# Performance work log

Measured on AMD Instinct MI355X. Metric: run time of the kernel, lower is better.

The kernel has to match this reference:

```python
import jax, jax.numpy as jnp
import numpy as np

EPSILON = 1e-6          # SwitchGate epsilon
CV_EPS = 1e-10          # cv_squared epsilon
CAPACITY_FACTOR = 1.0


def cv_squared(v):
    # torch: x.float().var() is unbiased (ddof=1) over the flattened tensor
    v = v.astype(jnp.float32).ravel()
    m = v.mean()
    return jnp.var(v, ddof=1) / (m * m + CV_EPS)


def setup_inputs() -> dict:
    key = jax.random.key(0)
    k1, k2 = jax.random.split(key, 2)
    B, N, D, E = 2048, 128, 512, 64
    x = jax.random.normal(k1, (B, N, D), dtype=jnp.float32)
    # nn.Linear(dim, num_experts): weight [E, D], bias [E]
    lim = 1.0 / (D ** 0.5)
    w_gate = jax.random.uniform(k2, (E, D), dtype=jnp.float32, minval=-lim, maxval=lim)
    b_gate = jnp.zeros((E,), dtype=jnp.float32)
    return {"x": x, "w_gate": w_gate, "b_gate": b_gate}


def reference(x, w_gate, b_gate):
    B, N, _ = x.shape
    E = w_gate.shape[0]
    capacity = int(CAPACITY_FACTOR * B)  # static

    logits = jnp.einsum('bnd,ed->bne', x, w_gate) + b_gate      # [B,N,E]
    gate_scores = jax.nn.softmax(logits, axis=-1)

    # topk(1, dim=-1) -> indices [B,N,1]
    _, idx = jax.lax.top_k(gate_scores, 1)

    # torch scatter_(dim=1, idx, 1): mask[b, idx[b,n,0], 0] = 1
    # (scatter along the SEQ dim with expert indices, faithful to source)
    bi = jnp.arange(B)[:, None]                                  # [B,1]
    mask = jnp.zeros_like(gate_scores).at[bi, idx[:, :, 0], 0].set(1.0)

    masked = gate_scores * mask                                  # [B,N,E]
    denom = masked.sum(axis=0, keepdims=True) + EPSILON          # [1,N,E]
    gs = masked / denom * capacity                               # [B,N,E]

    importance = gs.sum(axis=0)                                  # [N,E]
    load = (gs > 0).sum(axis=0)                                  # [N,E] int
    loss = cv_squared(importance) + cv_squared(load)
    return gs, loss
```

## Files before the change

kernel.cpp:

```cpp
#include <hip/hip_runtime.h>
#include <hip/hip_bf16.h>
#include <stdint.h>

#define Bb 2048
#define Nn 128
#define Dd 512
#define Ee 64
#define Mm (Bb * Nn)

typedef __bf16 bf16t;
typedef bf16t bf16x8 __attribute__((ext_vector_type(8)));
typedef float f32x4 __attribute__((ext_vector_type(4)));

union AFrag { bf16x8 v; uint32_t d[4]; };
union BFrag { bf16x8 v; uint4 q; };

__global__ __launch_bounds__(256) void k_packw(const float* __restrict__ w,
                                               uint16_t* __restrict__ whi,
                                               uint16_t* __restrict__ wlo) {
  int i = blockIdx.x * 256 + threadIdx.x;
  if (i < Ee * Dd) {
    float v = w[i];
    uint32_t ub = __float_as_uint(v);
    uint32_t h = ub >> 16;
    float rest = v - __uint_as_float(h << 16);
    whi[i] = (uint16_t)h;
    wlo[i] = (uint16_t)(__float_as_uint(rest) >> 16);
  }
}

__global__ __launch_bounds__(256) void k_main(const float* __restrict__ x,
    const uint16_t* __restrict__ whi, const uint16_t* __restrict__ wlo,
    const float* __restrict__ bg,
    float* __restrict__ out, float* __restrict__ gate0, int* __restrict__ amax)
{
  int tid = threadIdx.x;
  int wave = tid >> 6, lane = tid & 63;
  int l15 = lane & 15, quad = lane >> 4;

  {
    float4 z = make_float4(0.f, 0.f, 0.f, 0.f);
    float4* ob = (float4*)(out) + (size_t)blockIdx.x * 1024;
    #pragma unroll
    for (int i = 0; i < 4; ++i) ob[tid + 256 * i] = z;
  }

  size_t p0 = (size_t)blockIdx.x * 64 + (size_t)wave * 16;
  const float* xrow = x + (p0 + (size_t)l15) * Dd + quad * 8;

  f32x4 acc[4];
  #pragma unroll
  for (int ct = 0; ct < 4; ++ct) acc[ct] = (f32x4){0.f, 0.f, 0.f, 0.f};

  for (int kt = 0; kt < Dd; kt += 32) {
    float4 a0 = *(const float4*)(xrow + kt);
    float4 a1 = *(const float4*)(xrow + kt + 4);
    float av[8] = {a0.x, a0.y, a0.z, a0.w, a1.x, a1.y, a1.z, a1.w};
    AFrag ahi, alo;
    #pragma unroll
    for (int j = 0; j < 4; ++j) {
      uint32_t u0 = __float_as_uint(av[2 * j]);
      uint32_t u1 = __float_as_uint(av[2 * j + 1]);
      uint32_t h0 = u0 >> 16, h1 = u1 >> 16;
      float r0 = av[2 * j]     - __uint_as_float(h0 << 16);
      float r1 = av[2 * j + 1] - __uint_as_float(h1 << 16);
      uint32_t lo0 = __float_as_uint(r0) >> 16;
      uint32_t lo1 = __float_as_uint(r1) >> 16;
      ahi.d[j] = h0 | (h1 << 16);
      alo.d[j] = lo0 | (lo1 << 16);
    }
    #pragma unroll
    for (int ct = 0; ct < 4; ++ct) {
      int c = ct * 16 + l15;
      BFrag bh, bl;
      bh.q = *(const uint4*)(whi + (size_t)c * Dd + kt + quad * 8);
      bl.q = *(const uint4*)(wlo + (size_t)c * Dd + kt + quad * 8);
      acc[ct] = __builtin_amdgcn_mfma_f32_16x16x32_bf16(ahi.v, bh.v, acc[ct], 0, 0, 0);
      acc[ct] = __builtin_amdgcn_mfma_f32_16x16x32_bf16(ahi.v, bl.v, acc[ct], 0, 0, 0);
      acc[ct] = __builtin_amdgcn_mfma_f32_16x16x32_bf16(alo.v, bh.v, acc[ct], 0, 0, 0);
    }
  }

  float bia[4];
  #pragma unroll
  for (int ct = 0; ct < 4; ++ct) bia[ct] = bg[ct * 16 + l15];

  #pragma unroll
  for (int reg = 0; reg < 4; ++reg) {
    float v[4];
    #pragma unroll
    for (int ct = 0; ct < 4; ++ct) v[ct] = acc[ct][reg] + bia[ct];

    float mx = v[0]; int mi = l15;
    #pragma unroll
    for (int ct = 1; ct < 4; ++ct) {
      int c = ct * 16 + l15;
      if (v[ct] > mx) { mx = v[ct]; mi = c; }
    }
    #pragma unroll
    for (int off = 1; off < 16; off <<= 1) {
      float om = __shfl_xor(mx, off);
      int   oi = __shfl_xor(mi, off);
      if (om > mx || (om == mx && oi < mi)) { mx = om; mi = oi; }
    }
    float s = 0.f;
    #pragma unroll
    for (int ct = 0; ct < 4; ++ct) s += expf(v[ct] - mx);
    #pragma unroll
    for (int off = 1; off < 16; off <<= 1) s += __shfl_xor(s, off);

    if (l15 == 0) {
      size_t pr = p0 + (size_t)quad * 4 + reg;
      gate0[pr] = expf(v[0] - mx) / s;
      amax[pr]  = mi;
    }
  }
}

__global__ __launch_bounds__(64) void k_cov(const int* __restrict__ amax,
                                            const float* __restrict__ gate0,
                                            unsigned long long* __restrict__ covbits,
                                            float* __restrict__ covg) {
  int b = blockIdx.x;
  int lane = threadIdx.x;
  __shared__ int idxs[Nn];
  idxs[lane]      = amax[(size_t)b * Nn + lane];
  idxs[lane + 64] = amax[(size_t)b * Nn + 64 + lane];
  __syncthreads();
  bool cov = false;
  #pragma unroll 8
  for (int n = 0; n < Nn; ++n) cov |= (idxs[n] == lane);
  unsigned long long bits = __ballot(cov);
  if (lane == 0) covbits[b] = bits;
  covg[(size_t)b * Ee + lane] = cov ? gate0[(size_t)b * Nn + lane] : 0.f;
}

__global__ __launch_bounds__(256) void k_reduce(const float* __restrict__ covg,
                                                const unsigned long long* __restrict__ covbits,
                                                float* __restrict__ denomS,
                                                float* __restrict__ cntS) {
  int e = blockIdx.x;
  int t = threadIdx.x;
  float s = 0.f, c = 0.f;
  for (int b = t; b < Bb; b += 256) {
    s += covg[(size_t)b * Ee + e];
    c += (float)((covbits[b] >> e) & 1ull);
  }
  #pragma unroll
  for (int off = 1; off < 64; off <<= 1) {
    s += __shfl_xor(s, off);
    c += __shfl_xor(c, off);
  }
  __shared__ float ss[4], cs[4];
  int wave = t >> 6, lane = t & 63;
  if (lane == 0) { ss[wave] = s; cs[wave] = c; }
  __syncthreads();
  if (t == 0) {
    float S = 0.f, C = 0.f;
    #pragma unroll
    for (int i = 0; i < 4; ++i) { S += ss[i]; C += cs[i]; }
    denomS[e] = S;
    cntS[e] = C;
  }
}

__global__ __launch_bounds__(64) void k_scatter(const float* __restrict__ gate0,
                                                const unsigned long long* __restrict__ covbits,
                                                const float* __restrict__ denomS,
                                                float* __restrict__ out) {
  int b = blockIdx.x;
  int n = threadIdx.x;
  if ((covbits[b] >> n) & 1ull) {
    float g = gate0[(size_t)b * Nn + n];
    out[((size_t)(b * Nn + n)) * Ee] = g * 2048.0f / (denomS[n] + 1e-6f);
  }
}

__global__ __launch_bounds__(64) void k_loss(const float* __restrict__ denomS,
                                             const float* __restrict__ cntS,
                                             float* __restrict__ out) {
  int lane = threadIdx.x;
  double S = (double)denomS[lane];
  double imp = S / (S + 1e-6) * 2048.0;
  double ld = (double)cntS[lane];
  double s1i = imp, s2i = imp * imp, s1l = ld, s2l = ld * ld;
  #pragma unroll
  for (int off = 1; off < 64; off <<= 1) {
    s1i += __shfl_xor(s1i, off);
    s2i += __shfl_xor(s2i, off);
    s1l += __shfl_xor(s1l, off);
    s2l += __shfl_xor(s2l, off);
  }
  if (lane == 0) {
    const double Nt = (double)(Nn * Ee);
    double mi_ = s1i / Nt;
    double vi  = (s2i - Nt * mi_ * mi_) / (Nt - 1.0);
    double li  = vi / (mi_ * mi_ + 1e-10);
    double ml_ = s1l / Nt;
    double vl  = (s2l - Nt * ml_ * ml_) / (Nt - 1.0);
    double ll_ = vl / (ml_ * ml_ + 1e-10);
    out[(size_t)Mm * Ee] = (float)(li + ll_);
  }
}

extern "C" void kernel_launch(void* const* d_in, const int* in_sizes, int n_in,
                              void* d_out, int out_size, void* d_ws, size_t ws_size,
                              hipStream_t stream) {
  const float* x  = (const float*)d_in[0];
  const float* w  = (const float*)d_in[1];
  const float* bg = (const float*)d_in[2];
  float* out = (float*)d_out;

  char* ws = (char*)d_ws;
  float* gate0 = (float*)ws;
  int*   amax  = (int*)(ws + (size_t)Mm * 4);
  unsigned long long* covbits =
      (unsigned long long*)(ws + (size_t)Mm * 8);
  float* denomS = (float*)(ws + (size_t)Mm * 8 + (size_t)Bb * 8);
  float* cntS   = denomS + Ee;
  uint16_t* whi = (uint16_t*)(denomS + 2 * Ee);
  uint16_t* wlo = whi + Ee * Dd;
  float* covg   = (float*)(wlo + Ee * Dd);

  k_packw<<<(Ee * Dd + 255) / 256, 256, 0, stream>>>(w, whi, wlo);
  k_main<<<Mm / 64, 256, 0, stream>>>(x, whi, wlo, bg, out, gate0, amax);
  k_cov<<<Bb, 64, 0, stream>>>(amax, gate0, covbits, covg);
  k_reduce<<<Ee, 256, 0, stream>>>(covg, covbits, denomS, cntS);
  k_scatter<<<Bb, 64, 0, stream>>>(gate0, covbits, denomS, out);
  k_loss<<<1, 64, 0, stream>>>(denomS, cntS, out);
}
```

Before: 882.5 us.

## Tile four row groups per wave, reuse weight fragments, prefetch next x slice

Each wave now handles 64 rows (four 16-row tiles) instead of 16, so each weight hi/lo fragment loaded from global memory feeds four tiles of MFMAs. The x loads for the next k-step are software-prefetched into registers while the current step computes, and the fp32-to-bf16 hi/lo split uses byte-permute instructions. The grid shrinks by four and each block zeroes four times more output. Register pressure rises (16 accumulators plus prefetch buffers), which may lower occupancy. With only 1024 blocks, there is less parallelism for hiding the latency of this memory-bound x stream.

```diff
diff --git a/kernel.cpp b/kernel.cpp
--- a/kernel.cpp
+++ b/kernel.cpp
@@ -14,6 +14,14 @@
 
 union AFrag { bf16x8 v; uint32_t d[4]; };
 union BFrag { bf16x8 v; uint4 q; };
+
+__device__ __forceinline__ void split2(float f0, float f1, uint32_t& hi, uint32_t& lo) {
+  uint32_t u0 = __float_as_uint(f0), u1 = __float_as_uint(f1);
+  hi = __builtin_amdgcn_perm(u1, u0, 0x07060302u);
+  float r0 = f0 - __uint_as_float(u0 & 0xffff0000u);
+  float r1 = f1 - __uint_as_float(u1 & 0xffff0000u);
+  lo = __builtin_amdgcn_perm(__float_as_uint(r1), __float_as_uint(r0), 0x07060302u);
+}
 
 __global__ __launch_bounds__(256) void k_packw(const float* __restrict__ w,
                                                uint16_t* __restrict__ whi,
@@ -21,8 +29,7 @@
   int i = blockIdx.x * 256 + threadIdx.x;
   if (i < Ee * Dd) {
     float v = w[i];
-    uint32_t ub = __float_as_uint(v);
-    uint32_t h = ub >> 16;
+    uint32_t h = __float_as_uint(v) >> 16;
     float rest = v - __uint_as_float(h << 16);
     whi[i] = (uint16_t)h;
     wlo[i] = (uint16_t)(__float_as_uint(rest) >> 16);
@@ -40,44 +47,60 @@
 
   {
     float4 z = make_float4(0.f, 0.f, 0.f, 0.f);
-    float4* ob = (float4*)(out) + (size_t)blockIdx.x * 1024;
-    #pragma unroll
-    for (int i = 0; i < 4; ++i) ob[tid + 256 * i] = z;
-  }
-
-  size_t p0 = (size_t)blockIdx.x * 64 + (size_t)wave * 16;
-  const float* xrow = x + (p0 + (size_t)l15) * Dd + quad * 8;
-
-  f32x4 acc[4];
-  #pragma unroll
-  for (int ct = 0; ct < 4; ++ct) acc[ct] = (f32x4){0.f, 0.f, 0.f, 0.f};
+    float4* ob = (float4*)(out) + (size_t)blockIdx.x * 4096;
+    #pragma unroll
+    for (int i = 0; i < 16; ++i) ob[tid + 256 * i] = z;
+  }
+
+  size_t prow = (size_t)blockIdx.x * 256 + (size_t)wave * 64;
+  const float* xp = x + (prow + (size_t)l15) * Dd + quad * 8;
+
+  f32x4 acc[4][4];
+  #pragma unroll
+  for (int t = 0; t < 4; ++t)
+    #pragma unroll
+    for (int ct = 0; ct < 4; ++ct) acc[t][ct] = (f32x4){0.f, 0.f, 0.f, 0.f};
+
+  float4 an[4][2];
+  #pragma unroll
+  for (int t = 0; t < 4; ++t) {
+    an[t][0] = *(const float4*)(xp + t * 16 * Dd);
+    an[t][1] = *(const float4*)(xp + t * 16 * Dd + 4);
+  }
 
   for (int kt = 0; kt < Dd; kt += 32) {
-    float4 a0 = *(const float4*)(xrow + kt);
-    float4 a1 = *(const float4*)(xrow + kt + 4);
-    float av[8] = {a0.x, a0.y, a0.z, a0.w, a1.x, a1.y, a1.z, a1.w};
-    AFrag ahi, alo;
-    #pragma unroll
-    for (int j = 0; j < 4; ++j) {
-      uint32_t u0 = __float_as_uint(av[2 * j]);
-      uint32_t u1 = __float_as_uint(av[2 * j + 1]);
-      uint32_t h0 = u0 >> 16, h1 = u1 >> 16;
-      float r0 = av[2 * j]     - __uint_as_float(h0 << 16);
-      float r1 = av[2 * j + 1] - __uint_as_float(h1 << 16);
-      uint32_t lo0 = __float_as_uint(r0) >> 16;
-      uint32_t lo1 = __float_as_uint(r1) >> 16;
-      ahi.d[j] = h0 | (h1 << 16);
-      alo.d[j] = lo0 | (lo1 << 16);
-    }
+    int ktn = (kt + 32 < Dd) ? kt + 32 : 0;
+
+    BFrag bh[4], bl[4];
     #pragma unroll
     for (int ct = 0; ct < 4; ++ct) {
       int c = ct * 16 + l15;
-      BFrag bh, bl;
-      bh.q = *(const uint4*)(whi + (size_t)c * Dd + kt + quad * 8);
-      bl.q = *(const uint4*)(wlo + (size_t)c * Dd + kt + quad * 8);
-      acc[ct] = __builtin_amdgcn_mfma_f32_16x16x32_bf16(ahi.v, bh.v, acc[ct], 0, 0, 0);
-      acc[ct] = __builtin_amdgcn_mfma_f32_16x16x32_bf16(ahi.v, bl.v, acc[ct], 0, 0, 0);
-      acc[ct] = __builtin_amdgcn_mfma_f32_16x16x32_bf16(alo.v, bh.v, acc[ct], 0, 0, 0);
+      bh[ct].q = *(const uint4*)(whi + (size_t)c * Dd + kt + quad * 8);
+      bl[ct].q = *(const uint4*)(wlo + (size_t)c * Dd + kt + quad * 8);
+    }
+
+    float4 cur[4][2];
+    #pragma unroll
+    for (int t = 0; t < 4; ++t) { cur[t][0] = an[t][0]; cur[t][1] = an[t][1]; }
+    #pragma unroll
+    for (int t = 0; t < 4; ++t) {
+      an[t][0] = *(const float4*)(xp + t * 16 * Dd + ktn);
+      an[t][1] = *(const float4*)(xp + t * 16 * Dd + ktn + 4);
+    }
+
+    #pragma unroll
+    for (int t = 0; t < 4; ++t) {
+      AFrag ahi, alo;
+      split2(cur[t][0].x, cur[t][0].y, ahi.d[0], alo.d[0]);
+      split2(cur[t][0].z, cur[t][0].w, ahi.d[1], alo.d[1]);
+      split2(cur[t][1].x, cur[t][1].y, ahi.d[2], alo.d[2]);
+      split2(cur[t][1].z, cur[t][1].w, ahi.d[3], alo.d[3]);
+      #pragma unroll
+      for (int ct = 0; ct < 4; ++ct) {
+        acc[t][ct] = __builtin_amdgcn_mfma_f32_16x16x32_bf16(ahi.v, bh[ct].v, acc[t][ct], 0, 0, 0);
+        acc[t][ct] = __builtin_amdgcn_mfma_f32_16x16x32_bf16(ahi.v, bl[ct].v, acc[t][ct], 0, 0, 0);
+        acc[t][ct] = __builtin_amdgcn_mfma_f32_16x16x32_bf16(alo.v, bh[ct].v, acc[t][ct], 0, 0, 0);
+      }
     }
   }
 
@@ -86,33 +109,36 @@
   for (int ct = 0; ct < 4; ++ct) bia[ct] = bg[ct * 16 + l15];
 
   #pragma unroll
-  for (int reg = 0; reg < 4; ++reg) {
-    float v[4];
-    #pragma unroll
-    for (int ct = 0; ct < 4; ++ct) v[ct] = acc[ct][reg] + bia[ct];
-
-    float mx = v[0]; int mi = l15;
-    #pragma unroll
-    for (int ct = 1; ct < 4; ++ct) {
-      int c = ct * 16 + l15;
-      if (v[ct] > mx) { mx = v[ct]; mi = c; }
-    }
-    #pragma unroll
-    for (int off = 1; off < 16; off <<= 1) {
-      float om = __shfl_xor(mx, off);
-      int   oi = __shfl_xor(mi, off);
-      if (om > mx || (om == mx && oi < mi)) { mx = om; mi = oi; }
-    }
-    float s = 0.f;
-    #pragma unroll
-    for (int ct = 0; ct < 4; ++ct) s += expf(v[ct] - mx);
-    #pragma unroll
-    for (int off = 1; off < 16; off <<= 1) s += __shfl_xor(s, off);
-
-    if (l15 == 0) {
-      size_t pr = p0 + (size_t)quad * 4 + reg;
-      gate0[pr] = expf(v[0] - mx) / s;
-      amax[pr]  = mi;
+  for (int t = 0; t < 4; ++t) {
+    #pragma unroll
+    for (int reg = 0; reg < 4; ++reg) {
+      float v[4];
+      #pragma unroll
+      for (int ct = 0; ct < 4; ++ct) v[ct] = acc[t][ct][reg] + bia[ct];
+
+      float mx = v[0]; int mi = l15;
+      #pragma unroll
+      for (int ct = 1; ct < 4; ++ct) {
+        int c = ct * 16 + l15;
+        if (v[ct] > mx) { mx = v[ct]; mi = c; }
+      }
+      #pragma unroll
+      for (int off = 1; off < 16; off <<= 1) {
+        float om = __shfl_xor(mx, off);
+        int   oi = __shfl_xor(mi, off);
+        if (om > mx || (om == mx && oi < mi)) { mx = om; mi = oi; }
+      }
+      float s = 0.f;
+      #pragma unroll
+      for (int ct = 0; ct < 4; ++ct) s += expf(v[ct] - mx);
+      #pragma unroll
+      for (int off = 1; off < 16; off <<= 1) s += __shfl_xor(s, off);
+
+      if (l15 == 0) {
+        size_t pr = prow + (size_t)t * 16 + (size_t)quad * 4 + reg;
+        gate0[pr] = expf(v[0] - mx) / s;
+        amax[pr]  = mi;
+      }
     }
   }
 }
@@ -223,7 +249,7 @@
   float* covg   = (float*)(wlo + Ee * Dd);
 
   k_packw<<<(Ee * Dd + 255) / 256, 256, 0, stream>>>(w, whi, wlo);
-  k_main<<<Mm / 64, 256, 0, stream>>>(x, whi, wlo, bg, out, gate0, amax);
+  k_main<<<Mm / 256, 256, 0, stream>>>(x, whi, wlo, bg, out, gate0, amax);
   k_cov<<<Bb, 64, 0, stream>>>(amax, gate0, covbits, covg);
   k_reduce<<<Ee, 256, 0, stream>>>(covg, covbits, denomS, cntS);
   k_scatter<<<Bb, 64, 0, stream>>>(gate0, covbits, denomS, out);
```

Measured after the change: 754.8 us. 1.17x faster.
